# Kernel tuning notes

Measured on AMD Instinct MI355X. Metric: run time of the kernel, lower is better.

## Reference

```python
import jax, jax.numpy as jnp
import numpy as np

NUM_POS_FEATS = 512
LEN_EMBEDDING = 64


def setup_inputs() -> dict:
    key = jax.random.key(0)
    k1, k2 = jax.random.split(key)
    x = jax.random.normal(k1, (32, 3, 64, 64), dtype=jnp.float32)
    # nn.init.uniform_ -> U[0,1)
    row_embed = jax.random.uniform(k2, (LEN_EMBEDDING, NUM_POS_FEATS), dtype=jnp.float32)
    return {"x": x, "row_embed": row_embed}


def reference(x, row_embed):
    b = x.shape[0]
    h, w = x.shape[-2], x.shape[-1]
    center_x, center_y = w // 2, h // 2
    ii = jnp.arange(h)[:, None]   # row index i
    jj = jnp.arange(w)[None, :]   # col index j
    # shortest-path matrix: max(|cx - j| + |cy - i| - 1, 0)
    Z = jnp.maximum(jnp.abs(center_x - jj) + jnp.abs(center_y - ii) - 1, 0)  # [h, w] int
    pos = row_embed[Z]                          # [h, w, F] single fused gather
    pos = jnp.transpose(pos, (2, 0, 1))         # [F, h, w]
    pos = jnp.broadcast_to(pos[None], (b,) + pos.shape)  # [b, F, h, w]
    return pos
```

## Files before the change

### kernel.cpp

```cpp
#include <hip/hip_runtime.h>
#include <hip/hip_bf16.h>


#define NUM_POS_FEATS 512
#define H 64
#define W 64
#define B 32

__global__ __launch_bounds__(256) void pe_kernel(const float* __restrict__ row_embed,
                                                 float* __restrict__ out) {
    __shared__ float col[64];

    const int bf  = blockIdx.x;
    const int f   = bf & (NUM_POS_FEATS - 1);
    const int tid = threadIdx.x;

    if (tid < 64) {
        col[tid] = row_embed[tid * NUM_POS_FEATS + f];
    }
    __syncthreads();

    float4* o = reinterpret_cast<float4*>(out + (size_t)bf * (H * W));

#pragma unroll
    for (int k = 0; k < 4; ++k) {
        const int idx = k * 256 + tid;
        const int i   = idx >> 4;
        const int j4  = (idx & 15) << 2;
        const int di  = abs(32 - i);

        float4 v;
        {
            int z = di + abs(32 - (j4 + 0)) - 1; v.x = col[z < 0 ? 0 : z];
        }
        {
            int z = di + abs(32 - (j4 + 1)) - 1; v.y = col[z < 0 ? 0 : z];
        }
        {
            int z = di + abs(32 - (j4 + 2)) - 1; v.z = col[z < 0 ? 0 : z];
        }
        {
            int z = di + abs(32 - (j4 + 3)) - 1; v.w = col[z < 0 ? 0 : z];
        }
        o[idx] = v;
    }
}

extern "C" void kernel_launch(void* const* d_in, const int* in_sizes, int n_in,
                              void* d_out, int out_size, void* d_ws, size_t ws_size,
                              hipStream_t stream) {
    const float* row_embed = (const float*)d_in[1];
    float* out = (float*)d_out;

    const int grid = B * NUM_POS_FEATS;
    pe_kernel<<<grid, 256, 0, stream>>>(row_embed, out);
}
```

Measured before the change: 256.6 us.

## Compute each feature plane once and store it to all batches with nontemporal writes

The grid shrinks from B*F blocks to F blocks. Each block gathers and builds its 64x64 plane once, keeps it in registers, then loops over the 32 batch copies and writes each with nontemporal vector stores. This removes redundant shared-memory loads and index math per batch and is meant to bypass cache pollution on a pure write-bound kernel. The cost is fewer blocks (512) doing serial store loops, which could limit memory-level parallelism on a large GPU.

```diff
diff --git a/kernel.cpp b/kernel.cpp
--- a/kernel.cpp
+++ b/kernel.cpp
@@ -7,12 +7,13 @@
 #define W 64
 #define B 32
 
+typedef float vfloat4 __attribute__((ext_vector_type(4)));
+
 __global__ __launch_bounds__(256) void pe_kernel(const float* __restrict__ row_embed,
                                                  float* __restrict__ out) {
     __shared__ float col[64];
 
-    const int bf  = blockIdx.x;
-    const int f   = bf & (NUM_POS_FEATS - 1);
+    const int f   = blockIdx.x;
     const int tid = threadIdx.x;
 
     if (tid < 64) {
@@ -20,8 +21,7 @@
     }
     __syncthreads();
 
-    float4* o = reinterpret_cast<float4*>(out + (size_t)bf * (H * W));
-
+    vfloat4 v[4];
 #pragma unroll
     for (int k = 0; k < 4; ++k) {
         const int idx = k * 256 + tid;
@@ -29,20 +29,22 @@
         const int j4  = (idx & 15) << 2;
         const int di  = abs(32 - i);
 
-        float4 v;
-        {
-            int z = di + abs(32 - (j4 + 0)) - 1; v.x = col[z < 0 ? 0 : z];
+        int z0 = di + abs(32 - (j4 + 0)) - 1; z0 = z0 < 0 ? 0 : z0;
+        int z1 = di + abs(32 - (j4 + 1)) - 1; z1 = z1 < 0 ? 0 : z1;
+        int z2 = di + abs(32 - (j4 + 2)) - 1; z2 = z2 < 0 ? 0 : z2;
+        int z3 = di + abs(32 - (j4 + 3)) - 1; z3 = z3 < 0 ? 0 : z3;
+        v[k] = (vfloat4){col[z0], col[z1], col[z2], col[z3]};
+    }
+
+    vfloat4* obase = reinterpret_cast<vfloat4*>(out) + (size_t)f * (H * W / 4);
+    const size_t bstride = (size_t)NUM_POS_FEATS * (H * W / 4);
+
+    for (int b = 0; b < B; ++b) {
+        vfloat4* o = obase + (size_t)b * bstride;
+#pragma unroll
+        for (int k = 0; k < 4; ++k) {
+            __builtin_nontemporal_store(v[k], &o[k * 256 + tid]);
         }
-        {
-            int z = di + abs(32 - (j4 + 1)) - 1; v.y = col[z < 0 ? 0 : z];
-        }
-        {
-            int z = di + abs(32 - (j4 + 2)) - 1; v.z = col[z < 0 ? 0 : z];
-        }
-        {
-            int z = di + abs(32 - (j4 + 3)) - 1; v.w = col[z < 0 ? 0 : z];
-        }
-        o[idx] = v;
     }
 }
 
@@ -52,6 +54,5 @@
     const float* row_embed = (const float*)d_in[1];
     float* out = (float*)d_out;
 
-    const int grid = B * NUM_POS_FEATS;
-    pe_kernel<<<grid, 256, 0, stream>>>(row_embed, out);
+    pe_kernel<<<NUM_POS_FEATS, 256, 0, stream>>>(row_embed, out);
 }
```

Measured after the change: 266.5 us. 1.04x slower.
